# Kernel optimization log

Measured on AMD Instinct MI355X. Metric: run time of the kernel, lower is better.

Reference implementation:

```python
import jax, jax.numpy as jnp
import numpy as np

N = 1024          # sentence length
VW, DW = 100000, 300   # word vocab / embed dim
VP, DP = 64, 100       # pos vocab / embed dim
DV = DW + DP           # len_data_vec = 400 (LSTM in & hidden size)
H = 512                # MLP hidden
F = 128                # feature vec


def _lstm_dir(xs, h0, c0, Wih, Whh, bih, bhh):
    # PyTorch LSTM cell: gates ordered i, f, g, o
    def step(carry, x):
        h, c = carry
        g = x @ Wih.T + bih + h @ Whh.T + bhh
        i, f, gg, o = jnp.split(g, 4)
        i = jax.nn.sigmoid(i)
        f = jax.nn.sigmoid(f)
        gg = jnp.tanh(gg)
        o = jax.nn.sigmoid(o)
        c = f * c + i * gg
        h = o * jnp.tanh(c)
        return (h, c), h
    _, hs = jax.lax.scan(step, (h0, c0), xs)
    return hs  # [n, DV]


def setup_inputs() -> dict:
    key = jax.random.key(0)
    ks = jax.random.split(key, 24)
    s = 0.05
    inp = {
        'word_ids': jax.random.randint(ks[0], (N,), 0, VW),
        'pos_ids': jax.random.randint(ks[1], (N,), 0, VP),
        'h0': jax.random.normal(ks[2], (2, DV), jnp.float32),
        'c0': jax.random.normal(ks[3], (2, DV), jnp.float32),
        'word_emb': jax.random.normal(ks[4], (VW, DW), jnp.float32) * s,
        'pos_emb': jax.random.normal(ks[5], (VP, DP), jnp.float32) * s,
        'Wih_f': jax.random.normal(ks[6], (4 * DV, DV), jnp.float32) * s,
        'Whh_f': jax.random.normal(ks[7], (4 * DV, DV), jnp.float32) * s,
        'bih_f': jax.random.normal(ks[8], (4 * DV,), jnp.float32) * s,
        'bhh_f': jax.random.normal(ks[9], (4 * DV,), jnp.float32) * s,
        'Wih_b': jax.random.normal(ks[10], (4 * DV, DV), jnp.float32) * s,
        'Whh_b': jax.random.normal(ks[11], (4 * DV, DV), jnp.float32) * s,
        'bih_b': jax.random.normal(ks[12], (4 * DV,), jnp.float32) * s,
        'bhh_b': jax.random.normal(ks[13], (4 * DV,), jnp.float32) * s,
        'Wh1': jax.random.normal(ks[14], (H, 2 * DV), jnp.float32) * s,
        'bh1': jax.random.normal(ks[15], (H,), jnp.float32) * s,
        'Wh2': jax.random.normal(ks[16], (F, H), jnp.float32) * s,
        'bh2': jax.random.normal(ks[17], (F,), jnp.float32) * s,
        'Wd1': jax.random.normal(ks[18], (H, 2 * DV), jnp.float32) * s,
        'bd1': jax.random.normal(ks[19], (H,), jnp.float32) * s,
        'Wd2': jax.random.normal(ks[20], (F, H), jnp.float32) * s,
        'bd2': jax.random.normal(ks[21], (F,), jnp.float32) * s,
        'U_1': jax.random.normal(ks[22], (F, F), jnp.float32),
        'u_2': jax.random.normal(ks[23], (1, F), jnp.float32),
    }
    return inp


def reference(word_ids, pos_ids, h0, c0, word_emb, pos_emb,
              Wih_f, Whh_f, bih_f, bhh_f, Wih_b, Whh_b, bih_b, bhh_b,
              Wh1, bh1, Wh2, bh2, Wd1, bd1, Wd2, bd2, U_1, u_2):
    # Embedding gather + concat: x[i] = [word_emb; pos_emb]
    x = jnp.concatenate([word_emb[word_ids], pos_emb[pos_ids]], axis=-1)  # [n, DV]
    # BiLSTM (batch=1): forward dir and reversed dir, concat features
    r_f = _lstm_dir(x, h0[0], c0[0], Wih_f, Whh_f, bih_f, bhh_f)
    r_b = _lstm_dir(x[::-1], h0[1], c0[1], Wih_b, Whh_b, bih_b, bhh_b)[::-1]
    r = jnp.concatenate([r_f, r_b], axis=-1)  # [n, 2*DV]
    sr = jax.nn.sigmoid(r)
    # MLP_head / MLP_dep (clamp(min=0) == relu), batched over all tokens
    Hh = jax.nn.relu(sr @ Wh1.T + bh1) @ Wh2.T + bh2  # [n, F]
    Hd = jax.nn.relu(sr @ Wd1.T + bd1) @ Wd2.T + bd2  # [n, F]
    # Biaffine: adj[i,j] = h_i U h_j^T + h_i u_2^T
    adj = Hh @ U_1 @ Hd.T + Hh @ u_2.T  # [n, n] + [n, 1] broadcast
    return adj
```

## Files before the change

### kernel.cpp

```cpp
#include <hip/hip_runtime.h>
#include <math.h>

#define N_TOK 1024
#define DV    400
#define G4    1600
#define DWD   300
#define DPD   100
#define HID   512
#define FD    128
#define GWG   50
#define EPW   8

__device__ __forceinline__ float sigmoidf_(float x){ return 1.0f/(1.0f+__expf(-x)); }

__global__ void k_gather(const int* __restrict__ wid, const int* __restrict__ pid,
                         const float* __restrict__ wemb, const float* __restrict__ pemb,
                         float* __restrict__ x)
{
    int t = blockIdx.x;
    int w = wid[t], p = pid[t];
    for (int k = threadIdx.x; k < DV; k += blockDim.x){
        float v = (k < DWD) ? wemb[(long)w*DWD + k] : pemb[p*DPD + (k - DWD)];
        x[t*DV + k] = v;
    }
}

__global__ void k_transpose(const float* __restrict__ U, float* __restrict__ Ut, int n)
{
    int j = blockIdx.y*16 + threadIdx.y;
    int k = blockIdx.x*16 + threadIdx.x;
    if (j < n && k < n) Ut[j*n + k] = U[k*n + j];
}

__global__ __launch_bounds__(256) void k_gemm_nt(
    const float* __restrict__ A, const float* __restrict__ B,
    const float* __restrict__ bias1, const float* __restrict__ bias2,
    const float* __restrict__ rowbias, float* __restrict__ C,
    int M, int Nn, int K, int revA, int relu)
{
    const int BM = 64, BN = 64, BK = 16;
    __shared__ float As[BK][BM];
    __shared__ float Bs[BK][BN];
    int tid = threadIdx.x;
    int tx = tid & 15, ty = tid >> 4;
    int m0 = blockIdx.y*BM, n0 = blockIdx.x*BN;
    int lrow = tid >> 2;
    int lk   = (tid & 3) * 4;
    float acc[4][4] = {{0.f}};

    for (int k0 = 0; k0 < K; k0 += BK){
        int am = m0 + lrow; if (revA) am = M - 1 - am;
        const float4 av = *(const float4*)&A[(long)am*K + k0 + lk];
        const float4 bv = *(const float4*)&B[(long)(n0 + lrow)*K + k0 + lk];
        As[lk+0][lrow] = av.x; As[lk+1][lrow] = av.y; As[lk+2][lrow] = av.z; As[lk+3][lrow] = av.w;
        Bs[lk+0][lrow] = bv.x; Bs[lk+1][lrow] = bv.y; Bs[lk+2][lrow] = bv.z; Bs[lk+3][lrow] = bv.w;
        __syncthreads();
        #pragma unroll
        for (int kk = 0; kk < BK; ++kk){
            const float4 a = *(const float4*)&As[kk][ty*4];
            const float4 b = *(const float4*)&Bs[kk][tx*4];
            const float ar[4] = {a.x, a.y, a.z, a.w};
            const float br[4] = {b.x, b.y, b.z, b.w};
            #pragma unroll
            for (int i = 0; i < 4; ++i)
                #pragma unroll
                for (int j = 0; j < 4; ++j)
                    acc[i][j] += ar[i]*br[j];
        }
        __syncthreads();
    }

    #pragma unroll
    for (int i = 0; i < 4; ++i){
        int m = m0 + ty*4 + i;
        float rb = rowbias ? rowbias[m] : 0.0f;
        #pragma unroll
        for (int j = 0; j < 4; ++j){
            int n = n0 + tx*4 + j;
            float v = acc[i][j] + rb;
            if (bias1) v += bias1[n];
            if (bias2) v += bias2[n];
            if (relu)  v = fmaxf(v, 0.0f);
            C[(long)m*Nn + n] = v;
        }
    }
}

__global__ __launch_bounds__(256) void k_lstm(
    const float* __restrict__ Whh_f, const float* __restrict__ Whh_b,
    const float* __restrict__ Xf, const float* __restrict__ Xb,
    const float* __restrict__ h0, const float* __restrict__ c0,
    float* __restrict__ hf, float* __restrict__ hb,
    unsigned long long* __restrict__ mbox)
{
    __shared__ float W_s[32][DV];
    __shared__ float h_s[DV];

    int tid = threadIdx.x;
    int dir = blockIdx.x / GWG;
    int g   = blockIdx.x % GWG;
    int j0  = g * EPW;
    const float* Whh = dir ? Whh_b : Whh_f;
    const float* XX  = dir ? Xb    : Xf;
    float*       hout= dir ? hb    : hf;
    unsigned long long* mb = mbox + (size_t)dir * N_TOK * DV;

    for (int idx = tid; idx < 32*DV; idx += 256){
        int r = idx / DV, k = idx % DV;
        int grow = (r >> 3) * DV + j0 + (r & 7);
        W_s[r][k] = Whh[(long)grow*DV + k];
    }
    for (int idx = tid; idx < DV; idx += 256) h_s[idx] = h0[dir*DV + idx];

    int w    = tid >> 6;
    int lane = tid & 63;
    int q    = lane >> 4;
    int eo   = (lane >> 3) & 1;
    int l    = lane & 7;
    int e    = 2*w + eo;
    int r    = q*8 + e;
    int grow = q*DV + j0 + e;
    bool owner = (q == 0) && (l == 0);
    float c_reg = owner ? c0[dir*DV + j0 + e] : 0.0f;

    int s0 = tid;
    int s1 = 256 + tid;
    bool own0 = (s0 >= j0) && (s0 < j0 + EPW);
    bool own1 = (tid < 144) && (s1 >= j0) && (s1 < j0 + EPW);
    __syncthreads();

    float xv_n = 0.0f;
    if (l == 0) xv_n = XX[grow];

    bool dead = false;
    for (int t = 0; t < N_TOK; ++t){
        float xv = xv_n;

        float sum = 0.0f;
        const float2* wrow = (const float2*)&W_s[r][0];
        const float2* hp   = (const float2*)&h_s[0];
        #pragma unroll
        for (int i = 0; i < 25; ++i){
            float2 wv = wrow[l + 8*i];
            float2 hv = hp[l + 8*i];
            sum += wv.x*hv.x + wv.y*hv.y;
        }
        sum += __shfl_xor(sum, 1, 8);
        sum += __shfl_xor(sum, 2, 8);
        sum += __shfl_xor(sum, 4, 8);
        if (l == 0) sum += xv;

        float gi = __shfl(sum, eo*8 + 0,  64);
        float gf = __shfl(sum, eo*8 + 16, 64);
        float gg = __shfl(sum, eo*8 + 32, 64);
        float go = __shfl(sum, eo*8 + 48, 64);

        float h_new = 0.0f;
        if (owner){
            float iv = sigmoidf_(gi);
            float fv = sigmoidf_(gf);
            float gv = tanhf(gg);
            float ov = sigmoidf_(go);
            c_reg = fv*c_reg + iv*gv;
            h_new = ov * tanhf(c_reg);
            unsigned long long pk = (1ull << 32) | (unsigned long long)__float_as_uint(h_new);
            __hip_atomic_store(&mb[(size_t)t*DV + j0 + e], pk,
                               __ATOMIC_RELAXED, __HIP_MEMORY_SCOPE_AGENT);
            hout[(long)t*DV + j0 + e] = h_new;
        }

        __syncthreads();

        if (owner) h_s[j0 + e] = h_new;

        if (l == 0){
            int tn = (t + 1 < N_TOK) ? (t + 1) : t;
            xv_n = XX[(size_t)tn*G4 + grow];
        }

        const unsigned long long* mrow = &mb[(size_t)t*DV];
        float v0 = 0.0f, v1 = 0.0f;
        bool g0 = own0, g1 = own1 || (tid >= 144);
        if (!dead){
            int guard = 0;
            while (!(g0 && g1)){
                if (!g0){
                    unsigned long long u = __hip_atomic_load(&mrow[s0],
                                         __ATOMIC_RELAXED, __HIP_MEMORY_SCOPE_AGENT);
                    if (u >> 32){ v0 = __uint_as_float((unsigned)u); g0 = true; }
                }
                if (!g1){
                    unsigned long long u = __hip_atomic_load(&mrow[s1],
                                         __ATOMIC_RELAXED, __HIP_MEMORY_SCOPE_AGENT);
                    if (u >> 32){ v1 = __uint_as_float((unsigned)u); g1 = true; }
                }
                if (++guard > (1 << 16)) { dead = true; break; }
            }
            if (!own0 && g0) h_s[s0] = v0;
            if (tid < 144 && !own1 && g1) h_s[s1] = v1;
        }
        __syncthreads();
    }
}

__global__ void k_sr(const float* __restrict__ hf, const float* __restrict__ hb,
                     float* __restrict__ sr)
{
    int t = blockIdx.x;
    for (int c = threadIdx.x; c < 2*DV; c += blockDim.x){
        float v = (c < DV) ? hf[t*DV + c] : hb[(N_TOK-1-t)*DV + (c - DV)];
        sr[t*2*DV + c] = 1.0f/(1.0f+__expf(-v));
    }
}

__global__ void k_bvec(const float* __restrict__ Hh, const float* __restrict__ u2,
                       float* __restrict__ bvec)
{
    int i = blockIdx.x;
    int lane = threadIdx.x;
    float v = Hh[i*FD + lane]*u2[lane] + Hh[i*FD + 64 + lane]*u2[64 + lane];
    v += __shfl_xor(v, 1, 64);
    v += __shfl_xor(v, 2, 64);
    v += __shfl_xor(v, 4, 64);
    v += __shfl_xor(v, 8, 64);
    v += __shfl_xor(v, 16, 64);
    v += __shfl_xor(v, 32, 64);
    if (lane == 0) bvec[i] = v;
}

extern "C" void kernel_launch(void* const* d_in, const int* in_sizes, int n_in,
                              void* d_out, int out_size, void* d_ws, size_t ws_size,
                              hipStream_t stream)
{
    const int*   word_ids = (const int*)  d_in[0];
    const int*   pos_ids  = (const int*)  d_in[1];
    const float* h0    = (const float*)d_in[2];
    const float* c0    = (const float*)d_in[3];
    const float* wemb  = (const float*)d_in[4];
    const float* pemb  = (const float*)d_in[5];
    const float* Wih_f = (const float*)d_in[6];
    const float* Whh_f = (const float*)d_in[7];
    const float* bih_f = (const float*)d_in[8];
    const float* bhh_f = (const float*)d_in[9];
    const float* Wih_b = (const float*)d_in[10];
    const float* Whh_b = (const float*)d_in[11];
    const float* bih_b = (const float*)d_in[12];
    const float* bhh_b = (const float*)d_in[13];
    const float* Wh1   = (const float*)d_in[14];
    const float* bh1   = (const float*)d_in[15];
    const float* Wh2   = (const float*)d_in[16];
    const float* bh2   = (const float*)d_in[17];
    const float* Wd1   = (const float*)d_in[18];
    const float* bd1   = (const float*)d_in[19];
    const float* Wd2   = (const float*)d_in[20];
    const float* bd2   = (const float*)d_in[21];
    const float* U1    = (const float*)d_in[22];
    const float* u2    = (const float*)d_in[23];
    float* out = (float*)d_out;

    float* ws  = (float*)d_ws;
    float* x    = ws;
    float* Xf   = ws + 409600;
    float* Xb   = ws + 2048000;
    float* hf   = ws + 3686400;
    float* hb   = ws + 4096000;
    float* sr   = ws + 4505600;
    float* T1h  = ws + 5324800;
    float* T1d  = ws + 5849088;
    float* Hh   = ws + 6373376;
    float* Hd   = ws + 6504448;
    float* G1   = ws + 6635520;
    float* Ut   = ws + 6766592;
    float* bvec = ws + 6782976;
    unsigned long long* mbox = (unsigned long long*)(ws + 4505600);

    hipMemsetAsync(mbox, 0, (size_t)2*N_TOK*DV*sizeof(unsigned long long), stream);

    k_gather<<<N_TOK, 128, 0, stream>>>(word_ids, pos_ids, wemb, pemb, x);
    k_transpose<<<dim3(8,8), dim3(16,16), 0, stream>>>(U1, Ut, FD);

    dim3 blk(256);
    k_gemm_nt<<<dim3(G4/64, N_TOK/64), blk, 0, stream>>>(x, Wih_f, bih_f, bhh_f, nullptr, Xf,
                                                         N_TOK, G4, DV, 0, 0);
    k_gemm_nt<<<dim3(G4/64, N_TOK/64), blk, 0, stream>>>(x, Wih_b, bih_b, bhh_b, nullptr, Xb,
                                                         N_TOK, G4, DV, 1, 0);
    k_lstm<<<2*GWG, 256, 0, stream>>>(Whh_f, Whh_b, Xf, Xb, h0, c0, hf, hb, mbox);

    k_sr<<<N_TOK, 256, 0, stream>>>(hf, hb, sr);

    k_gemm_nt<<<dim3(HID/64, N_TOK/64), blk, 0, stream>>>(sr, Wh1, bh1, nullptr, nullptr, T1h,
                                                          N_TOK, HID, 2*DV, 0, 1);
    k_gemm_nt<<<dim3(HID/64, N_TOK/64), blk, 0, stream>>>(sr, Wd1, bd1, nullptr, nullptr, T1d,
                                                          N_TOK, HID, 2*DV, 0, 1);
    k_gemm_nt<<<dim3(FD/64,  N_TOK/64), blk, 0, stream>>>(T1h, Wh2, bh2, nullptr, nullptr, Hh,
                                                          N_TOK, FD, HID, 0, 0);
    k_gemm_nt<<<dim3(FD/64,  N_TOK/64), blk, 0, stream>>>(T1d, Wd2, bd2, nullptr, nullptr, Hd,
                                                          N_TOK, FD, HID, 0, 0);
    k_bvec<<<N_TOK, 64, 0, stream>>>(Hh, u2, bvec);
    k_gemm_nt<<<dim3(FD/64,  N_TOK/64), blk, 0, stream>>>(Hh, Ut, nullptr, nullptr, nullptr, G1,
                                                          N_TOK, FD, FD, 0, 0);
    k_gemm_nt<<<dim3(N_TOK/64, N_TOK/64), blk, 0, stream>>>(G1, Hd, nullptr, nullptr, bvec, out,
                                                            N_TOK, N_TOK, FD, 0, 0);
}
```

Measured before the change: 2.655 ms.

## Keep LSTM recurrent weights in registers, double-buffer h, pipeline mailbox polling

The recurrent LSTM kernel now holds each thread's slice of Whh in registers instead of shared memory. It double-buffers the hidden state so one __syncthreads per step can be removed. It also issues the mailbox atomic loads for the next hidden values early, as three in-flight loads per slot, so polling latency overlaps the matvec, and it prefetches the input-projection value earlier. The cost is higher register pressure (launch bounds set to one block per CU) and extra speculative global loads per step.

```diff
diff --git a/kernel.cpp b/kernel.cpp
--- a/kernel.cpp
+++ b/kernel.cpp
@@ -12,6 +12,8 @@
 #define EPW   8
 
 __device__ __forceinline__ float sigmoidf_(float x){ return 1.0f/(1.0f+__expf(-x)); }
+
+#define LDA(p) __hip_atomic_load((p), __ATOMIC_RELAXED, __HIP_MEMORY_SCOPE_AGENT)
 
 __global__ void k_gather(const int* __restrict__ wid, const int* __restrict__ pid,
                          const float* __restrict__ wemb, const float* __restrict__ pemb,
@@ -86,15 +88,15 @@
     }
 }
 
-__global__ __launch_bounds__(256) void k_lstm(
+__global__ __launch_bounds__(256, 1) void k_lstm(
     const float* __restrict__ Whh_f, const float* __restrict__ Whh_b,
     const float* __restrict__ Xf, const float* __restrict__ Xb,
     const float* __restrict__ h0, const float* __restrict__ c0,
     float* __restrict__ hf, float* __restrict__ hb,
     unsigned long long* __restrict__ mbox)
 {
-    __shared__ float W_s[32][DV];
-    __shared__ float h_s[DV];
+    __shared__ float hA[DV];
+    __shared__ float hB[DV];
 
     int tid = threadIdx.x;
     int dir = blockIdx.x / GWG;
@@ -105,28 +107,31 @@
     float*       hout= dir ? hb    : hf;
     unsigned long long* mb = mbox + (size_t)dir * N_TOK * DV;
 
-    for (int idx = tid; idx < 32*DV; idx += 256){
-        int r = idx / DV, k = idx % DV;
-        int grow = (r >> 3) * DV + j0 + (r & 7);
-        W_s[r][k] = Whh[(long)grow*DV + k];
-    }
-    for (int idx = tid; idx < DV; idx += 256) h_s[idx] = h0[dir*DV + idx];
-
     int w    = tid >> 6;
     int lane = tid & 63;
     int q    = lane >> 4;
     int eo   = (lane >> 3) & 1;
     int l    = lane & 7;
     int e    = 2*w + eo;
-    int r    = q*8 + e;
     int grow = q*DV + j0 + e;
     bool owner = (q == 0) && (l == 0);
     float c_reg = owner ? c0[dir*DV + j0 + e] : 0.0f;
+
+    float2 wreg[25];
+    {
+        const float* wrow = Whh + (size_t)grow * DV;
+        #pragma unroll
+        for (int i = 0; i < 25; ++i)
+            wreg[i] = *(const float2*)&wrow[2*l + 16*i];
+    }
+
+    for (int idx = tid; idx < DV; idx += 256) hA[idx] = h0[dir*DV + idx];
 
     int s0 = tid;
     int s1 = 256 + tid;
     bool own0 = (s0 >= j0) && (s0 < j0 + EPW);
     bool own1 = (tid < 144) && (s1 >= j0) && (s1 < j0 + EPW);
+    bool skip1 = own1 || (tid >= 144);
     __syncthreads();
 
     float xv_n = 0.0f;
@@ -134,16 +139,26 @@
 
     bool dead = false;
     for (int t = 0; t < N_TOK; ++t){
+        const unsigned long long* mrow = &mb[(size_t)t*DV];
+        const unsigned long long* p0 = &mrow[s0];
+        const unsigned long long* p1 = (tid < 144) ? &mrow[s1] : p0;
+
+        unsigned long long q0a = LDA(p0), q1a = LDA(p1);
+        unsigned long long q0b = LDA(p0), q1b = LDA(p1);
+        unsigned long long q0c = LDA(p0), q1c = LDA(p1);
+
         float xv = xv_n;
-
+        if (l == 0){
+            int tn = (t + 1 < N_TOK) ? (t + 1) : t;
+            xv_n = XX[(size_t)tn*G4 + grow];
+        }
+
+        const float2* hc2 = (const float2*)((t & 1) ? hB : hA);
         float sum = 0.0f;
-        const float2* wrow = (const float2*)&W_s[r][0];
-        const float2* hp   = (const float2*)&h_s[0];
         #pragma unroll
         for (int i = 0; i < 25; ++i){
-            float2 wv = wrow[l + 8*i];
-            float2 hv = hp[l + 8*i];
-            sum += wv.x*hv.x + wv.y*hv.y;
+            float2 hv = hc2[l + 8*i];
+            sum += wreg[i].x*hv.x + wreg[i].y*hv.y;
         }
         sum += __shfl_xor(sum, 1, 8);
         sum += __shfl_xor(sum, 2, 8);
@@ -155,49 +170,36 @@
         float gg = __shfl(sum, eo*8 + 32, 64);
         float go = __shfl(sum, eo*8 + 48, 64);
 
-        float h_new = 0.0f;
+        float* hn = (t & 1) ? hA : hB;
+
         if (owner){
             float iv = sigmoidf_(gi);
             float fv = sigmoidf_(gf);
             float gv = tanhf(gg);
             float ov = sigmoidf_(go);
             c_reg = fv*c_reg + iv*gv;
-            h_new = ov * tanhf(c_reg);
+            float h_new = ov * tanhf(c_reg);
             unsigned long long pk = (1ull << 32) | (unsigned long long)__float_as_uint(h_new);
             __hip_atomic_store(&mb[(size_t)t*DV + j0 + e], pk,
                                __ATOMIC_RELAXED, __HIP_MEMORY_SCOPE_AGENT);
             hout[(long)t*DV + j0 + e] = h_new;
-        }
-
-        __syncthreads();
-
-        if (owner) h_s[j0 + e] = h_new;
-
-        if (l == 0){
-            int tn = (t + 1 < N_TOK) ? (t + 1) : t;
-            xv_n = XX[(size_t)tn*G4 + grow];
-        }
-
-        const unsigned long long* mrow = &mb[(size_t)t*DV];
-        float v0 = 0.0f, v1 = 0.0f;
-        bool g0 = own0, g1 = own1 || (tid >= 144);
+            hn[j0 + e] = h_new;
+        }
+
         if (!dead){
+            bool g0 = own0, g1 = skip1;
             int guard = 0;
             while (!(g0 && g1)){
                 if (!g0){
-                    unsigned long long u = __hip_atomic_load(&mrow[s0],
-                                         __ATOMIC_RELAXED, __HIP_MEMORY_SCOPE_AGENT);
-                    if (u >> 32){ v0 = __uint_as_float((unsigned)u); g0 = true; }
+                    if (q0a >> 32){ hn[s0] = __uint_as_float((unsigned)q0a); g0 = true; }
+                    else { q0a = q0b; q0b = q0c; q0c = LDA(p0); }
                 }
                 if (!g1){
-                    unsigned long long u = __hip_atomic_load(&mrow[s1],
-                                         __ATOMIC_RELAXED, __HIP_MEMORY_SCOPE_AGENT);
-                    if (u >> 32){ v1 = __uint_as_float((unsigned)u); g1 = true; }
+                    if (q1a >> 32){ hn[s1] = __uint_as_float((unsigned)q1a); g1 = true; }
+                    else { q1a = q1b; q1b = q1c; q1c = LDA(p1); }
                 }
-                if (++guard > (1 << 16)) { dead = true; break; }
+                if (++guard > (1 << 18)) { dead = true; break; }
             }
-            if (!own0 && g0) h_s[s0] = v0;
-            if (tid < 144 && !own1 && g1) h_s[s1] = v1;
         }
         __syncthreads();
     }
```

Result: slower. 3.325 ms (+25.3%).
